# Kernel optimization log

Measured on AMD Instinct MI355X. Metric: run time of the kernel, lower is better.

Reference implementation:

```python
import jax, jax.numpy as jnp
import numpy as np

HIDDEN = 2048
Q_HEADS = 16
KV_HEADS = 4
HEAD_DIM = HIDDEN // Q_HEADS  # 128
GROUPS = Q_HEADS // KV_HEADS  # 4


def setup_inputs() -> dict:
    key = jax.random.key(0)
    ks = jax.random.split(key, 5)
    scale = 1.0 / np.sqrt(HIDDEN)
    x = jax.random.normal(ks[0], (1, 4096, HIDDEN), dtype=jnp.float32)
    # nn.Linear weights stored as [out_features, in_features]
    Wq = jax.random.uniform(ks[1], (Q_HEADS * HEAD_DIM, HIDDEN), jnp.float32, -scale, scale)
    Wk = jax.random.uniform(ks[2], (KV_HEADS * HEAD_DIM, HIDDEN), jnp.float32, -scale, scale)
    Wv = jax.random.uniform(ks[3], (KV_HEADS * HEAD_DIM, HIDDEN), jnp.float32, -scale, scale)
    Wo = jax.random.uniform(ks[4], (HIDDEN, HIDDEN), jnp.float32, -scale, scale)
    return {"x": x, "Wq": Wq, "Wk": Wk, "Wv": Wv, "Wo": Wo}


def reference(x, Wq, Wk, Wv, Wo):
    b, s, _ = x.shape
    norm = jnp.asarray(np.sqrt(HEAD_DIM), x.dtype)
    # Projections (Linear without bias: x @ W.T)
    q = (x @ Wq.T).reshape(b, s, KV_HEADS, GROUPS, HEAD_DIM)  # group q heads by shared kv head
    k = (x @ Wk.T).reshape(b, s, KV_HEADS, HEAD_DIM)
    v = (x @ Wv.T).reshape(b, s, KV_HEADS, HEAD_DIM)
    # Scores: repeat_interleave of KV is equivalent to sharing k across the g axis
    att = jnp.einsum('bskgd,btkd->bkgst', q, k) / norm  # [b,kv,groups,s,s]
    att = jax.nn.softmax(att, axis=-1)
    out = jnp.einsum('bkgst,btkd->bskgd', att, v).reshape(b, s, HIDDEN)
    return out @ Wo.T
```

## Files before the change

### kernel.cpp

```cpp
#include <hip/hip_runtime.h>
#include <stdint.h>

#define SEQ 4096
#define HID 2048

typedef __attribute__((ext_vector_type(8))) short short8;
typedef __attribute__((ext_vector_type(4))) float f32x4;
typedef __attribute__((ext_vector_type(16))) float f32x16;
typedef unsigned int u32;
typedef __attribute__((ext_vector_type(4))) u32 u32x4;

__device__ __forceinline__ short bf16_rne(float f) {
  u32 u = __builtin_bit_cast(u32, f);
  u += 0x7FFFu + ((u >> 16) & 1u);
  return (short)(u >> 16);
}

__device__ __forceinline__ void gload16(const void* gp, void* lp) {
  __builtin_amdgcn_global_load_lds(
      (const __attribute__((address_space(1))) u32*)(uintptr_t)gp,
      (__attribute__((address_space(3))) u32*)(uintptr_t)lp, 16, 0, 0);
}

__global__ __launch_bounds__(256) void cast_bf16(const float* __restrict__ in,
                                                 short* __restrict__ out, int n8) {
  int i = blockIdx.x * 256 + threadIdx.x;
  if (i >= n8) return;
  const f32x4* p = (const f32x4*)in + (size_t)i * 2;
  f32x4 a = p[0], b = p[1];
  short8 o;
#pragma unroll
  for (int j = 0; j < 4; ++j) { o[j] = bf16_rne(a[j]); o[j + 4] = bf16_rne(b[j]); }
  *((short8*)out + i) = o;
}

__global__ __launch_bounds__(256) void transpose_v(const short* __restrict__ qkv,
                                                   short* __restrict__ vt) {
  __shared__ __align__(16) short tile[64][72];
  int rb = blockIdx.x * 64, cb = blockIdx.y * 64;
  int tid = threadIdx.x;
  int tr = tid >> 3, tc = (tid & 7) * 8;
#pragma unroll
  for (int i = 0; i < 2; ++i)
    *(short8*)&tile[tr + i * 32][tc] =
        *(const short8*)&qkv[(size_t)(rb + tr + i * 32) * 3072 + 2560 + cb + tc];
  __syncthreads();
#pragma unroll
  for (int i = 0; i < 2; ++i) {
    int c = tr + i * 32;
    short8 v;
#pragma unroll
    for (int j = 0; j < 8; ++j) v[j] = tile[tc + j][c];
    *(short8*)&vt[(size_t)(cb + c) * SEQ + rb + tc] = v;
  }
}

template <typename CT>
__global__ __launch_bounds__(256, 2) void gemm_nt(const short* __restrict__ A,
                                                  const short* __restrict__ B,
                                                  CT* __restrict__ C, int M, int N, int K) {
  __shared__ __align__(16) short As[128 * 32];
  __shared__ __align__(16) short Bs[128 * 32];
  int tid = threadIdx.x, wave = tid >> 6, lane = tid & 63;
  int lr = lane & 15, lg = lane >> 4;
  int wr = wave >> 1, wc = wave & 1;
  size_t rowA0 = (size_t)blockIdx.y * 128, colB0 = (size_t)blockIdx.x * 128;
  f32x4 acc[4][4] = {};

  for (int kt = 0; kt < K; kt += 32) {
#pragma unroll
    for (int c = 0; c < 2; ++c) {
      int chunk = wave * 2 + c;
      int row = chunk * 16 + (lane >> 2);
      int col = (lane & 3) * 8;
      gload16(A + (rowA0 + row) * (size_t)K + kt + col, &As[chunk * 512]);
      gload16(B + (colB0 + row) * (size_t)K + kt + col, &Bs[chunk * 512]);
    }
    __syncthreads();
    short8 a[4], b[4];
#pragma unroll
    for (int i = 0; i < 4; ++i) {
      a[i] = *(const short8*)&As[(wr * 64 + i * 16 + lr) * 32 + lg * 8];
      b[i] = *(const short8*)&Bs[(wc * 64 + i * 16 + lr) * 32 + lg * 8];
    }
#pragma unroll
    for (int i = 0; i < 4; ++i)
#pragma unroll
      for (int j = 0; j < 4; ++j)
        acc[i][j] = __builtin_amdgcn_mfma_f32_16x16x32_bf16(a[i], b[j], acc[i][j], 0, 0, 0);
    __syncthreads();
  }
#pragma unroll
  for (int i = 0; i < 4; ++i)
#pragma unroll
    for (int j = 0; j < 4; ++j)
#pragma unroll
      for (int r = 0; r < 4; ++r) {
        size_t row = rowA0 + wr * 64 + i * 16 + lg * 4 + r;
        size_t col = colB0 + wc * 64 + j * 16 + lr;
        if constexpr (sizeof(CT) == 2) C[row * N + col] = (CT)bf16_rne(acc[i][j][r]);
        else C[row * N + col] = acc[i][j][r];
      }
}

__global__ __launch_bounds__(256, 2) void attn_kernel(const short* __restrict__ QKV,
                                                      const short* __restrict__ Vt,
                                                      short* __restrict__ Oat) {
  __shared__ __align__(16) short Ks[2][4096];
  __shared__ __align__(16) short Vs[2][4096];
  int tid = threadIdx.x, wave = tid >> 6, lane = tid & 63;
  int l31 = lane & 31, hi = lane >> 5;
  int h = blockIdx.y, kv = h >> 2;
  int q0 = blockIdx.x * 128 + wave * 32;

  short8 qf[8];
#pragma unroll
  for (int kb = 0; kb < 8; ++kb)
    qf[kb] = *(const short8*)&QKV[(size_t)(q0 + l31) * 3072 + h * 128 + kb * 16 + hi * 8];

  f32x16 oacc[4] = {};
  float m_run = -1e30f, lsum = 0.f;

  const float sc = 1.44269504089f * 0.08838834764831845f;
  const float THR_S = 60.f;
  const short* Kbase = QKV + 2048 + kv * 128;

  auto stageK = [&](int b, int t0) {
#pragma unroll
    for (int cc = 0; cc < 2; ++cc) {
      int c = wave * 2 + cc;
      gload16(Kbase + (size_t)(t0 + l31) * 3072 + c * 16 + hi * 8, &Ks[b][c * 512]);
    }
  };
  auto stageV = [&](int b, int t0) {
#pragma unroll
    for (int cc = 0; cc < 2; ++cc) {
      int c = wave * 2 + cc;
      int d = (c & 1) * 64 + lane;
      gload16(Vt + (size_t)(kv * 128 + d) * SEQ + t0 + (c >> 1) * 8, &Vs[b][c * 512]);
    }
  };

  stageK(0, 0);
  stageV(0, 0);
  __syncthreads();
  int buf = 0;

  for (int t0 = 0; t0 < SEQ; t0 += 32) {
    int tn = (t0 + 32 < SEQ) ? t0 + 32 : 0;
    stageK(buf ^ 1, tn);
    stageV(buf ^ 1, tn);

    f32x16 sacc = {};
    __builtin_amdgcn_s_setprio(1);
#pragma unroll
    for (int kb = 0; kb < 8; ++kb) {
      short8 kf = *(const short8*)&Ks[buf][((kb * 2 + hi) * 32 + l31) * 8];
      sacc = __builtin_amdgcn_mfma_f32_32x32x16_bf16(kf, qf[kb], sacc, 0, 0, 0);
    }
    __builtin_amdgcn_s_setprio(0);

    float vmax = fmaxf(sacc[0], sacc[1]);
#pragma unroll
    for (int r = 2; r < 16; ++r) vmax = fmaxf(vmax, sacc[r]);
    if (__any(vmax > m_run + THR_S)) {
      float mnew = fmaxf(fmaxf(vmax, __shfl_xor(vmax, 32)), m_run);
      float corr = __builtin_amdgcn_exp2f((m_run - mnew) * sc);
      lsum *= corr;
      m_run = mnew;
#pragma unroll
      for (int nb = 0; nb < 4; ++nb) oacc[nb] *= corr;
    }

    float p[16];
    float ps = 0.f;
#pragma unroll
    for (int r = 0; r < 16; ++r) {
      p[r] = __builtin_amdgcn_exp2f((sacc[r] - m_run) * sc);
      ps += p[r];
    }
    lsum += ps;
    u32 w[8];
#pragma unroll
    for (int i = 0; i < 8; ++i)
      asm("v_cvt_pk_bf16_f32 %0, %1, %2" : "=v"(w[i]) : "v"(p[2 * i]), "v"(p[2 * i + 1]));

    u32 W[8];
#pragma unroll
    for (int i = 0; i < 2; ++i) {
      u32 ex = __shfl_xor(hi ? w[i] : w[i + 2], 32);
      W[i] = hi ? ex : w[i];
      W[i + 2] = hi ? w[i + 2] : ex;
      u32 ex2 = __shfl_xor(hi ? w[i + 4] : w[i + 6], 32);
      W[i + 4] = hi ? ex2 : w[i + 4];
      W[i + 6] = hi ? w[i + 6] : ex2;
    }
    short8 pa0 = __builtin_bit_cast(short8, (u32x4){W[0], W[1], W[2], W[3]});
    short8 pa1 = __builtin_bit_cast(short8, (u32x4){W[4], W[5], W[6], W[7]});

    __builtin_amdgcn_s_setprio(1);
#pragma unroll
    for (int nb = 0; nb < 4; ++nb) {
      short8 v0 = *(const short8*)&Vs[buf][((hi)*128 + nb * 32 + l31) * 8];
      oacc[nb] = __builtin_amdgcn_mfma_f32_32x32x16_bf16(pa0, v0, oacc[nb], 0, 0, 0);
      short8 v1 = *(const short8*)&Vs[buf][((2 + hi) * 128 + nb * 32 + l31) * 8];
      oacc[nb] = __builtin_amdgcn_mfma_f32_32x32x16_bf16(pa1, v1, oacc[nb], 0, 0, 0);
    }
    __builtin_amdgcn_s_setprio(0);

    __syncthreads();
    buf ^= 1;
  }

  lsum += __shfl_xor(lsum, 32);
  float linv = 1.f / lsum;
#pragma unroll
  for (int r = 0; r < 16; ++r) {
    int qrow = (r & 3) + 8 * (r >> 2) + 4 * hi;
    float lr_ = __shfl(linv, qrow);
#pragma unroll
    for (int nb = 0; nb < 4; ++nb)
      Oat[(size_t)(q0 + qrow) * HID + h * 128 + nb * 32 + l31] = bf16_rne(oacc[nb][r] * lr_);
  }
}

extern "C" void kernel_launch(void* const* d_in, const int* in_sizes, int n_in,
                              void* d_out, int out_size, void* d_ws, size_t ws_size,
                              hipStream_t stream) {
  const float* x = (const float*)d_in[0];
  const float* Wq = (const float*)d_in[1];
  const float* Wk = (const float*)d_in[2];
  const float* Wv = (const float*)d_in[3];
  const float* Wo = (const float*)d_in[4];
  float* out = (float*)d_out;
  char* ws = (char*)d_ws;

  short* xb = (short*)(ws);
  short* wqkv = (short*)(ws + (16u << 20));
  short* wob = (short*)(ws + (28u << 20));
  short* qkv = (short*)(ws + (36u << 20));
  short* vt = wqkv;
  short* oat = xb;

  cast_bf16<<<4096, 256, 0, stream>>>(x, xb, 1048576);
  cast_bf16<<<2048, 256, 0, stream>>>(Wq, wqkv, 524288);
  cast_bf16<<<512, 256, 0, stream>>>(Wk, wqkv + (size_t)2048 * 2048, 131072);
  cast_bf16<<<512, 256, 0, stream>>>(Wv, wqkv + (size_t)2560 * 2048, 131072);
  cast_bf16<<<2048, 256, 0, stream>>>(Wo, wob, 524288);

  gemm_nt<short><<<dim3(24, 32), 256, 0, stream>>>(xb, wqkv, qkv, 4096, 3072, 2048);
  transpose_v<<<dim3(64, 8), 256, 0, stream>>>(qkv, vt);
  attn_kernel<<<dim3(32, 16), 256, 0, stream>>>(qkv, vt, oat);
  gemm_nt<float><<<dim3(16, 32), 256, 0, stream>>>(oat, wob, out, 4096, HID, 2048);
}
```

Measured before the change: 294.2 us.

## Split attention KV range across two blocks and merge partials

Attention now runs as a split-K style pass: each (q-tile, head) is processed by two blocks covering half the key range each. Each block writes fp16 partial outputs plus its running max and sum, and a new merge kernel combines them into the bf16 attention output. This doubles the grid from 512 to 1024 blocks for better CU occupancy, and raises launch bounds to 4 blocks per CU. The V transpose now permutes token order within groups of 16 so the P-matrix cross-lane shuffles can be dropped. The exp is also rewritten as a fused multiply-subtract. The cost is extra global traffic for the partials, an extra kernel launch, and a workspace-size dependency for the split path.

```diff
diff --git a/kernel.cpp b/kernel.cpp
--- a/kernel.cpp
+++ b/kernel.cpp
@@ -5,6 +5,7 @@
 #define HID 2048
 
 typedef __attribute__((ext_vector_type(8))) short short8;
+typedef __attribute__((ext_vector_type(8))) _Float16 half8;
 typedef __attribute__((ext_vector_type(4))) float f32x4;
 typedef __attribute__((ext_vector_type(16))) float f32x16;
 typedef unsigned int u32;
@@ -50,7 +51,11 @@
     int c = tr + i * 32;
     short8 v;
 #pragma unroll
-    for (int j = 0; j < 8; ++j) v[j] = tile[tc + j][c];
+    for (int j = 0; j < 8; ++j) {
+      int pos = tc + j;
+      int tl = (pos & ~15) | (pos & 3) | ((pos & 4) << 1) | ((pos & 8) >> 1);
+      v[j] = tile[tl][c];
+    }
     *(short8*)&vt[(size_t)(cb + c) * SEQ + rb + tc] = v;
   }
 }
@@ -103,14 +108,18 @@
       }
 }
 
-__global__ __launch_bounds__(256, 2) void attn_kernel(const short* __restrict__ QKV,
+template <int NSPLIT>
+__global__ __launch_bounds__(256, 4) void attn_kernel(const short* __restrict__ QKV,
                                                       const short* __restrict__ Vt,
-                                                      short* __restrict__ Oat) {
+                                                      short* __restrict__ Oat,
+                                                      _Float16* __restrict__ Op,
+                                                      float* __restrict__ ml) {
   __shared__ __align__(16) short Ks[2][4096];
   __shared__ __align__(16) short Vs[2][4096];
   int tid = threadIdx.x, wave = tid >> 6, lane = tid & 63;
   int l31 = lane & 31, hi = lane >> 5;
   int h = blockIdx.y, kv = h >> 2;
+  int part = (NSPLIT == 2) ? blockIdx.z : 0;
   int q0 = blockIdx.x * 128 + wave * 32;
 
   short8 qf[8];
@@ -141,13 +150,16 @@
     }
   };
 
-  stageK(0, 0);
-  stageV(0, 0);
+  const int tbeg = part * (SEQ / NSPLIT);
+  const int tend = tbeg + SEQ / NSPLIT;
+
+  stageK(0, tbeg);
+  stageV(0, tbeg);
   __syncthreads();
   int buf = 0;
 
-  for (int t0 = 0; t0 < SEQ; t0 += 32) {
-    int tn = (t0 + 32 < SEQ) ? t0 + 32 : 0;
+  for (int t0 = tbeg; t0 < tend; t0 += 32) {
+    int tn = (t0 + 32 < tend) ? t0 + 32 : tbeg;
     stageK(buf ^ 1, tn);
     stageV(buf ^ 1, tn);
 
@@ -172,31 +184,19 @@
       for (int nb = 0; nb < 4; ++nb) oacc[nb] *= corr;
     }
 
-    float p[16];
+    float msc = m_run * sc;
     float ps = 0.f;
-#pragma unroll
-    for (int r = 0; r < 16; ++r) {
-      p[r] = __builtin_amdgcn_exp2f((sacc[r] - m_run) * sc);
-      ps += p[r];
+    u32 w[8];
+#pragma unroll
+    for (int i = 0; i < 8; ++i) {
+      float p0 = __builtin_amdgcn_exp2f(sacc[2 * i] * sc - msc);
+      float p1 = __builtin_amdgcn_exp2f(sacc[2 * i + 1] * sc - msc);
+      ps += p0 + p1;
+      asm("v_cvt_pk_bf16_f32 %0, %1, %2" : "=v"(w[i]) : "v"(p0), "v"(p1));
     }
     lsum += ps;
-    u32 w[8];
-#pragma unroll
-    for (int i = 0; i < 8; ++i)
-      asm("v_cvt_pk_bf16_f32 %0, %1, %2" : "=v"(w[i]) : "v"(p[2 * i]), "v"(p[2 * i + 1]));
-
-    u32 W[8];
-#pragma unroll
-    for (int i = 0; i < 2; ++i) {
-      u32 ex = __shfl_xor(hi ? w[i] : w[i + 2], 32);
-      W[i] = hi ? ex : w[i];
-      W[i + 2] = hi ? w[i + 2] : ex;
-      u32 ex2 = __shfl_xor(hi ? w[i + 4] : w[i + 6], 32);
-      W[i + 4] = hi ? ex2 : w[i + 4];
-      W[i + 6] = hi ? w[i + 6] : ex2;
-    }
-    short8 pa0 = __builtin_bit_cast(short8, (u32x4){W[0], W[1], W[2], W[3]});
-    short8 pa1 = __builtin_bit_cast(short8, (u32x4){W[4], W[5], W[6], W[7]});
+    short8 pa0 = __builtin_bit_cast(short8, (u32x4){w[0], w[1], w[2], w[3]});
+    short8 pa1 = __builtin_bit_cast(short8, (u32x4){w[4], w[5], w[6], w[7]});
 
     __builtin_amdgcn_s_setprio(1);
 #pragma unroll
@@ -213,15 +213,56 @@
   }
 
   lsum += __shfl_xor(lsum, 32);
-  float linv = 1.f / lsum;
-#pragma unroll
-  for (int r = 0; r < 16; ++r) {
-    int qrow = (r & 3) + 8 * (r >> 2) + 4 * hi;
-    float lr_ = __shfl(linv, qrow);
-#pragma unroll
-    for (int nb = 0; nb < 4; ++nb)
-      Oat[(size_t)(q0 + qrow) * HID + h * 128 + nb * 32 + l31] = bf16_rne(oacc[nb][r] * lr_);
-  }
+
+  if constexpr (NSPLIT == 1) {
+    float linv = 1.f / lsum;
+#pragma unroll
+    for (int r = 0; r < 16; ++r) {
+      int qrow = (r & 3) + 8 * (r >> 2) + 4 * hi;
+      float lr_ = __shfl(linv, qrow);
+#pragma unroll
+      for (int nb = 0; nb < 4; ++nb)
+        Oat[(size_t)(q0 + qrow) * HID + h * 128 + nb * 32 + l31] = bf16_rne(oacc[nb][r] * lr_);
+    }
+  } else {
+    _Float16* Obase = Op + (size_t)part * SEQ * HID;
+#pragma unroll
+    for (int r = 0; r < 16; ++r) {
+      int qrow = (r & 3) + 8 * (r >> 2) + 4 * hi;
+#pragma unroll
+      for (int nb = 0; nb < 4; ++nb)
+        Obase[(size_t)(q0 + qrow) * HID + h * 128 + nb * 32 + l31] = (_Float16)oacc[nb][r];
+    }
+    if (hi == 0) {
+      size_t base = (((size_t)part * SEQ + q0 + l31) * 16 + h) * 2;
+      ml[base] = m_run;
+      ml[base + 1] = lsum;
+    }
+  }
+}
+
+__global__ __launch_bounds__(256) void merge_parts(const _Float16* __restrict__ Op,
+                                                   const float* __restrict__ ml,
+                                                   short* __restrict__ Oat) {
+  const float sc = 1.44269504089f * 0.08838834764831845f;
+  int i = blockIdx.x * 256 + threadIdx.x;
+  int row = i >> 8;
+  int col = (i & 255) * 8;
+  int h = col >> 7;
+  const float* a = ml + (((size_t)row) * 16 + h) * 2;
+  const float* b = ml + (((size_t)SEQ + row) * 16 + h) * 2;
+  float m1 = a[0], l1 = a[1], m2 = b[0], l2 = b[1];
+  float M = fmaxf(m1, m2);
+  float e1 = __builtin_amdgcn_exp2f((m1 - M) * sc);
+  float e2 = __builtin_amdgcn_exp2f((m2 - M) * sc);
+  float inv = 1.f / (l1 * e1 + l2 * e2);
+  half8 o1 = *(const half8*)&Op[(size_t)row * HID + col];
+  half8 o2 = *(const half8*)&Op[(size_t)SEQ * HID + (size_t)row * HID + col];
+  short8 o;
+#pragma unroll
+  for (int j = 0; j < 8; ++j)
+    o[j] = bf16_rne(((float)o1[j] * e1 + (float)o2[j] * e2) * inv);
+  *(short8*)&Oat[(size_t)row * HID + col] = o;
 }
 
 extern "C" void kernel_launch(void* const* d_in, const int* in_sizes, int n_in,
@@ -241,6 +282,9 @@
   short* qkv = (short*)(ws + (36u << 20));
   short* vt = wqkv;
   short* oat = xb;
+  _Float16* opart = (_Float16*)(ws + 62914560u);
+  float* mlb = (float*)(ws + 62914560u + 33554432u);
+  const bool split = ws_size >= (size_t)(62914560u + 33554432u + 1048576u);
 
   cast_bf16<<<4096, 256, 0, stream>>>(x, xb, 1048576);
   cast_bf16<<<2048, 256, 0, stream>>>(Wq, wqkv, 524288);
@@ -250,6 +294,11 @@
 
   gemm_nt<short><<<dim3(24, 32), 256, 0, stream>>>(xb, wqkv, qkv, 4096, 3072, 2048);
   transpose_v<<<dim3(64, 8), 256, 0, stream>>>(qkv, vt);
-  attn_kernel<<<dim3(32, 16), 256, 0, stream>>>(qkv, vt, oat);
+  if (split) {
+    attn_kernel<2><<<dim3(32, 16, 2), 256, 0, stream>>>(qkv, vt, nullptr, opart, mlb);
+    merge_parts<<<4096, 256, 0, stream>>>(opart, mlb, oat);
+  } else {
+    attn_kernel<1><<<dim3(32, 16, 1), 256, 0, stream>>>(qkv, vt, oat, nullptr, nullptr);
+  }
   gemm_nt<float><<<dim3(16, 32), 256, 0, stream>>>(oat, wob, out, 4096, HID, 2048);
 }
```

After: 459.1 us. 56.1% more time.
